# Kernel tuning notes

Hardware: AMD Instinct MI355X
Metric: run time of the kernel (lower is better)

Reference implementation:

```python
import jax, jax.numpy as jnp
import numpy as np
from jax.scipy.special import logsumexp

SEQ, BATCH, NUM_TAGS = 1024, 512, 64


def setup_inputs() -> dict:
    key = jax.random.key(0)
    k_em, k_tag, k_len, k_s, k_e, k_t = jax.random.split(key, 6)
    emissions = jax.random.normal(k_em, (SEQ, BATCH, NUM_TAGS), dtype=jnp.float32)
    tags = jax.random.randint(k_tag, (SEQ, BATCH), 0, NUM_TAGS, dtype=jnp.int64)
    # random sequence lengths in [1, SEQ]; mask[0] is guaranteed all ones
    lengths = jax.random.randint(k_len, (BATCH,), 1, SEQ + 1)
    mask = (jnp.arange(SEQ)[:, None] < lengths[None, :]).astype(jnp.int32)
    # CRF params: uniform(-0.1, 0.1) as in reset_parameters()
    u = lambda k, shape: jax.random.uniform(k, shape, jnp.float32, -0.1, 0.1)
    return {
        "emissions": emissions,
        "tags": tags,
        "mask": mask,
        "start_transitions": u(k_s, (NUM_TAGS,)),
        "end_transitions": u(k_e, (NUM_TAGS,)),
        "transitions": u(k_t, (NUM_TAGS, NUM_TAGS)),
    }


def _compute_score(emissions, tags, maskf, start_transitions, end_transitions, transitions):
    # emissions: (S,B,T), tags/maskf: (S,B)
    S, B = tags.shape
    em_scores = jnp.take_along_axis(emissions, tags[:, :, None], axis=2)[..., 0]  # (S,B)
    trans_scores = transitions[tags[:-1], tags[1:]]  # (S-1,B)
    score = start_transitions[tags[0]] + em_scores[0]
    score = score + jnp.sum((trans_scores + em_scores[1:]) * maskf[1:], axis=0)
    seq_ends = maskf.astype(jnp.int32).sum(axis=0) - 1  # (B,)
    last_tags = tags[seq_ends, jnp.arange(B)]
    return score + end_transitions[last_tags]


def _compute_normalizer(emissions, mask, start_transitions, end_transitions, transitions):
    # forward algorithm: sequential logsumexp scan over timesteps
    def step(score, x):  # score: (B,T)
        em_t, m_t = x  # (B,T), (B,)
        nxt = logsumexp(score[:, :, None] + transitions[None, :, :] + em_t[:, None, :], axis=1)
        score = jnp.where(m_t[:, None] > 0, nxt, score)
        return score, None

    score0 = start_transitions[None, :] + emissions[0]  # (B,T)
    score, _ = jax.lax.scan(step, score0, (emissions[1:], mask[1:]))
    return logsumexp(score + end_transitions[None, :], axis=1)  # (B,)


def reference(emissions, tags, mask, start_transitions, end_transitions, transitions):
    maskf = mask.astype(emissions.dtype)
    numerator = _compute_score(emissions, tags, maskf, start_transitions, end_transitions, transitions)
    denominator = _compute_normalizer(emissions, mask, start_transitions, end_transitions, transitions)
    llh = numerator - denominator
    return llh.sum()  # reduction='sum' (default)
```

## Files before the change

### kernel.cpp

```cpp
#include <hip/hip_runtime.h>
#include <stdint.h>

#define SEQ 1024
#define BATCH 512
#define NTAGS 64
#define HALF_T 512
#define LOGD 4.158883083f

typedef _Float16 v2h   __attribute__((ext_vector_type(2)));
typedef float    f32x4 __attribute__((ext_vector_type(4)));

__device__ __forceinline__ float dot2acc(v2h a, v2h b, float c) {
#if __has_builtin(__builtin_amdgcn_fdot2)
    return __builtin_amdgcn_fdot2(a, b, c, false);
#else
    return fmaf((float)a.x, (float)b.x, fmaf((float)a.y, (float)b.y, c));
#endif
}

__device__ __forceinline__ float rfl(float x) {
    return __uint_as_float(__builtin_amdgcn_readfirstlane(__float_as_uint(x)));
}

__device__ __forceinline__ v2h bch(float f) { return __builtin_bit_cast(v2h, f); }

__global__ __launch_bounds__(128)
void crf_kernel(const float* __restrict__ em,
                const int* __restrict__ tags,
                const int* __restrict__ mask,
                const float* __restrict__ startT,
                const float* __restrict__ endT,
                const float* __restrict__ trans,
                float* __restrict__ out)
{
    const int  b   = blockIdx.x;
    const int  wid = threadIdx.x >> 6;
    const int  j   = threadIdx.x & 63;
    const bool fwd = (wid == 0);

    __shared__ __align__(16) _Float16 bsh[2][NTAGS];
    __shared__ float gsh[NTAGS];
    __shared__ float mb_np[2];

    const unsigned lbase = (unsigned)(uintptr_t)(&bsh[wid][0]);
    const unsigned wa    = lbase + 2u * (unsigned)j;
    const unsigned ra    = lbase;

    int lsum = 0;
#pragma unroll
    for (int k = 0; k < SEQ / 64; ++k)
        lsum += mask[(k * 64 + j) * BATCH + b];
#pragma unroll
    for (int off = 32; off > 0; off >>= 1)
        lsum += __shfl_xor(lsum, off);
    const int L = lsum;

    v2h w[32];
#pragma unroll
    for (int i = 0; i < 32; ++i) {
        float a0, a1;
        if (fwd) { a0 = trans[(2 * i) * NTAGS + j]; a1 = trans[(2 * i + 1) * NTAGS + j]; }
        else     { a0 = trans[j * NTAGS + 2 * i];   a1 = trans[j * NTAGS + 2 * i + 1];   }
        v2h t; t.x = (_Float16)__expf(a0); t.y = (_Float16)__expf(a1);
        w[i] = t;
    }

#define DOT(WRVAL, SOUT)                                                         \
    {                                                                            \
        f32x4 q0, q1, q2, q3, q4, q5, q6, q7;                                    \
        float vtmp;                                                              \
        asm volatile(                                                            \
            "v_cvt_f16_f32 %[t], %[v]\n\t"                                       \
            "ds_write_b16 %[wa], %[t]\n\t"                                       \
            "ds_read_b128 %[a0], %[ra] offset:0\n\t"                             \
            "ds_read_b128 %[a1], %[ra] offset:16\n\t"                            \
            "ds_read_b128 %[a2], %[ra] offset:32\n\t"                            \
            "ds_read_b128 %[a3], %[ra] offset:48\n\t"                            \
            "ds_read_b128 %[a4], %[ra] offset:64\n\t"                            \
            "ds_read_b128 %[a5], %[ra] offset:80\n\t"                            \
            "ds_read_b128 %[a6], %[ra] offset:96\n\t"                            \
            "ds_read_b128 %[a7], %[ra] offset:112\n\t"                           \
            "s_waitcnt lgkmcnt(4)"                                               \
            : [a0] "=&v"(q0), [a1] "=&v"(q1), [a2] "=&v"(q2), [a3] "=&v"(q3),    \
              [a4] "=&v"(q4), [a5] "=&v"(q5), [a6] "=&v"(q6), [a7] "=&v"(q7),    \
              [t] "=&v"(vtmp)                                                    \
            : [v] "v"(WRVAL), [wa] "v"(wa), [ra] "v"(ra));                       \
        __builtin_amdgcn_sched_barrier(0);                                       \
        float s0 = 0.f, s1 = 0.f, s2 = 0.f, s3 = 0.f;                            \
        s0 = dot2acc(bch(q0.x), w[0],  s0);                                      \
        s1 = dot2acc(bch(q1.x), w[4],  s1);                                      \
        s2 = dot2acc(bch(q2.x), w[8],  s2);                                      \
        s3 = dot2acc(bch(q3.x), w[12], s3);                                      \
        s0 = dot2acc(bch(q0.y), w[1],  s0);                                      \
        s1 = dot2acc(bch(q1.y), w[5],  s1);                                      \
        s2 = dot2acc(bch(q2.y), w[9],  s2);                                      \
        s3 = dot2acc(bch(q3.y), w[13], s3);                                      \
        s0 = dot2acc(bch(q0.z), w[2],  s0);                                      \
        s1 = dot2acc(bch(q1.z), w[6],  s1);                                      \
        s2 = dot2acc(bch(q2.z), w[10], s2);                                      \
        s3 = dot2acc(bch(q3.z), w[14], s3);                                      \
        s0 = dot2acc(bch(q0.w), w[3],  s0);                                      \
        s1 = dot2acc(bch(q1.w), w[7],  s1);                                      \
        s2 = dot2acc(bch(q2.w), w[11], s2);                                      \
        s3 = dot2acc(bch(q3.w), w[15], s3);                                      \
        asm volatile("s_waitcnt lgkmcnt(0)"                                      \
                     : "+v"(q4), "+v"(q5), "+v"(q6), "+v"(q7));                  \
        __builtin_amdgcn_sched_barrier(0);                                       \
        float s4 = 0.f, s5 = 0.f, s6 = 0.f, s7 = 0.f;                            \
        s4 = dot2acc(bch(q4.x), w[16], s4);                                      \
        s5 = dot2acc(bch(q5.x), w[20], s5);                                      \
        s6 = dot2acc(bch(q6.x), w[24], s6);                                      \
        s7 = dot2acc(bch(q7.x), w[28], s7);                                      \
        s4 = dot2acc(bch(q4.y), w[17], s4);                                      \
        s5 = dot2acc(bch(q5.y), w[21], s5);                                      \
        s6 = dot2acc(bch(q6.y), w[25], s6);                                      \
        s7 = dot2acc(bch(q7.y), w[29], s7);                                      \
        s4 = dot2acc(bch(q4.z), w[18], s4);                                      \
        s5 = dot2acc(bch(q5.z), w[22], s5);                                      \
        s6 = dot2acc(bch(q6.z), w[26], s6);                                      \
        s7 = dot2acc(bch(q7.z), w[30], s7);                                      \
        s4 = dot2acc(bch(q4.w), w[19], s4);                                      \
        s5 = dot2acc(bch(q5.w), w[23], s5);                                      \
        s6 = dot2acc(bch(q6.w), w[27], s6);                                      \
        s7 = dot2acc(bch(q7.w), w[31], s7);                                      \
        SOUT = ((s0 + s1) + (s2 + s3)) + ((s4 + s5) + (s6 + s7));                \
    }

    float beta, M;
    int nsteps = 0;

    if (fwd) {
        float em0 = em[(size_t)b * NTAGS + j];
        float a0  = startT[j] + em0;
        M    = __shfl(a0, 0);
        beta = __expf(a0 - M);

        const int Lf = min(L - 1, HALF_T - 1);
        int t = 1;
        float cur[4], nxt[4];
#pragma unroll
        for (int u = 0; u < 4; ++u) {
            cur[u] = em[((size_t)min(t + u,     SEQ - 1) * BATCH + b) * NTAGS + j];
            nxt[u] = em[((size_t)min(t + 4 + u, SEQ - 1) * BATCH + b) * NTAGS + j];
        }
        while (t + 3 <= Lf) {
            float pre[4];
#pragma unroll
            for (int u = 0; u < 4; ++u)
                pre[u] = em[((size_t)min(t + 8 + u, SEQ - 1) * BATCH + b) * NTAGS + j];
            float eem[4];
#pragma unroll
            for (int u = 0; u < 4; ++u) eem[u] = __expf(cur[u] - LOGD);

            float s;
            DOT(beta, s); beta = s * eem[0];
            DOT(beta, s);
            float r = rfl(s);
            beta = s * eem[1];
            DOT(beta, s); beta = s * eem[2];
            float rinv = 1.0f / r;
            float lr   = __logf(r);
            DOT(beta, s); beta = s * (eem[3] * rinv);
            M += lr;
            nsteps += 4;
#pragma unroll
            for (int u = 0; u < 4; ++u) { cur[u] = nxt[u]; nxt[u] = pre[u]; }
            t += 4;
        }
        for (; t <= Lf; ++t) {
            float emt = em[((size_t)t * BATCH + b) * NTAGS + j];
            float s; DOT(beta, s);
            beta = s * __expf(emt - LOGD);
            ++nsteps;
        }
    } else {
        beta = __expf(endT[j]);
        M = 0.0f;
        if (L - 1 >= HALF_T) {
            int tt = L - 1;
            float cur[4], nxt[4];
#pragma unroll
            for (int u = 0; u < 4; ++u) {
                cur[u] = em[((size_t)max(tt - u,     0) * BATCH + b) * NTAGS + j];
                nxt[u] = em[((size_t)max(tt - 4 - u, 0) * BATCH + b) * NTAGS + j];
            }
            while (tt - 3 >= HALF_T) {
                float pre[4];
#pragma unroll
                for (int u = 0; u < 4; ++u)
                    pre[u] = em[((size_t)max(tt - 8 - u, 0) * BATCH + b) * NTAGS + j];
                float eem[4];
#pragma unroll
                for (int u = 0; u < 4; ++u) eem[u] = __expf(cur[u] - LOGD);

                float s;
                DOT(beta * eem[0], s); beta = s;
                DOT(beta * eem[1], s);
                float r = rfl(s);
                beta = s;
                DOT(beta * eem[2], s); beta = s;
                float rinv = 1.0f / r;
                float lr   = __logf(r);
                DOT(beta * (eem[3] * rinv), s); beta = s;
                M += lr;
                nsteps += 4;
#pragma unroll
                for (int u = 0; u < 4; ++u) { cur[u] = nxt[u]; nxt[u] = pre[u]; }
                tt -= 4;
            }
            for (; tt >= HALF_T; --tt) {
                float emt = em[((size_t)tt * BATCH + b) * NTAGS + j];
                float s; DOT(beta * __expf(emt - LOGD), s);
                beta = s;
                ++nsteps;
            }
        }
    }
#undef DOT

    const float Mfb = fmaf((float)nsteps, LOGD, M);

    if (!fwd) {
        gsh[j] = beta;
        if (j == 0) mb_np[0] = Mfb;
    }

    float np = 0.0f;
#pragma unroll
    for (int k = 0; k < SEQ / 128; ++k) {
        int t = k * 128 + wid * 64 + j;
        if (t >= 1 && t < L) {
            int ct = tags[t * BATCH + b];
            int pt = tags[(t - 1) * BATCH + b];
            np += trans[pt * NTAGS + ct] + em[((size_t)t * BATCH + b) * NTAGS + ct];
        }
    }
    if (threadIdx.x == 0) {
        int t0 = tags[b];
        np += startT[t0] + em[(size_t)b * NTAGS + t0]
            + endT[tags[(size_t)(L - 1) * BATCH + b]];
    }
#pragma unroll
    for (int off = 32; off > 0; off >>= 1)
        np += __shfl_xor(np, off);
    if (!fwd && j == 0) mb_np[1] = np;

    __syncthreads();

    if (fwd) {
        float p = beta * gsh[j];
#pragma unroll
        for (int off = 32; off > 0; off >>= 1)
            p += __shfl_xor(p, off);
        if (j == 0) {
            float denom = __logf(p) + Mfb + mb_np[0];
            atomicAdd(out, (np + mb_np[1]) - denom);
        }
    }
}

extern "C" void kernel_launch(void* const* d_in, const int* in_sizes, int n_in,
                              void* d_out, int out_size, void* d_ws, size_t ws_size,
                              hipStream_t stream)
{
    const float* em     = (const float*)d_in[0];
    const int*   tags   = (const int*)d_in[1];
    const int*   mask   = (const int*)d_in[2];
    const float* startT = (const float*)d_in[3];
    const float* endT   = (const float*)d_in[4];
    const float* trans  = (const float*)d_in[5];
    float*       out    = (float*)d_out;

    (void)d_ws; (void)ws_size;

    hipMemsetAsync(out, 0, sizeof(float) * out_size, stream);
    crf_kernel<<<BATCH, 128, 0, stream>>>(em, tags, mask, startT, endT, trans, out);
}
```

Baseline: 308.4 us.

## Replace LDS broadcast of alpha vector with cross-lane DPP/permlane expansion

The per-step all-to-all broadcast of the 64-wide scaled score vector, previously done with an LDS write and eight 128-bit LDS reads, now runs entirely in registers. It uses permlane32/16 swaps, packed fp16 conversion and a tree of DPP moves. Each lane gets its own permuted ordering of source tags, so the transition weights are loaded with a matching index permutation. This removes LDS latency and waits from the serial recurrence, at the cost of about 30 dependent DPP instructions per step and some extra register pressure.

Result: slower. 348.9 us (+13.1%).

```diff
diff --git a/kernel.cpp b/kernel.cpp
--- a/kernel.cpp
+++ b/kernel.cpp
@@ -1,5 +1,4 @@
 #include <hip/hip_runtime.h>
-#include <stdint.h>
 
 #define SEQ 1024
 #define BATCH 512
@@ -7,8 +6,7 @@
 #define HALF_T 512
 #define LOGD 4.158883083f
 
-typedef _Float16 v2h   __attribute__((ext_vector_type(2)));
-typedef float    f32x4 __attribute__((ext_vector_type(4)));
+typedef _Float16 v2h __attribute__((ext_vector_type(2)));
 
 __device__ __forceinline__ float dot2acc(v2h a, v2h b, float c) {
 #if __has_builtin(__builtin_amdgcn_fdot2)
@@ -22,7 +20,56 @@
     return __uint_as_float(__builtin_amdgcn_readfirstlane(__float_as_uint(x)));
 }
 
-__device__ __forceinline__ v2h bch(float f) { return __builtin_bit_cast(v2h, f); }
+template<int CTRL>
+__device__ __forceinline__ unsigned dppmov(unsigned v) {
+    return (unsigned)__builtin_amdgcn_mov_dpp((int)v, CTRL, 0xf, 0xf, false);
+}
+
+__device__ __forceinline__ void swap32pair(unsigned x, unsigned& a, unsigned& b) {
+#if __has_builtin(__builtin_amdgcn_permlane32_swap)
+    auto r = __builtin_amdgcn_permlane32_swap(x, x, false, false);
+    a = (unsigned)r[0]; b = (unsigned)r[1];
+#else
+    a = x; b = (unsigned)__shfl_xor((int)x, 32);
+#endif
+}
+
+__device__ __forceinline__ void swap16pair(unsigned x, unsigned& a, unsigned& b) {
+#if __has_builtin(__builtin_amdgcn_permlane16_swap)
+    auto r = __builtin_amdgcn_permlane16_swap(x, x, false, false);
+    a = (unsigned)r[0]; b = (unsigned)r[1];
+#else
+    a = x; b = (unsigned)__shfl_xor((int)x, 16);
+#endif
+}
+
+__device__ __forceinline__ void expand64(unsigned p0, unsigned u[32]) {
+    swap16pair(p0, u[0], u[1]);
+    u[2] = dppmov<0x140>(u[0]);
+    u[3] = dppmov<0x140>(u[1]);
+#pragma unroll
+    for (int k = 0; k < 4; ++k)  u[4 + k]  = dppmov<0x141>(u[k]);
+#pragma unroll
+    for (int k = 0; k < 8; ++k)  u[8 + k]  = dppmov<0x4E>(u[k]);
+#pragma unroll
+    for (int k = 0; k < 16; ++k) u[16 + k] = dppmov<0xB1>(u[k]);
+}
+
+__device__ __forceinline__ void bcast64(float x, v2h p[32]) {
+    unsigned a, b;
+    swap32pair(__float_as_uint(x), a, b);
+#if __has_builtin(__builtin_amdgcn_cvt_pkrtz)
+    auto pk_ = __builtin_amdgcn_cvt_pkrtz(__uint_as_float(a), __uint_as_float(b));
+    unsigned pk = __builtin_bit_cast(unsigned, pk_);
+#else
+    v2h pkv; pkv.x = (_Float16)__uint_as_float(a); pkv.y = (_Float16)__uint_as_float(b);
+    unsigned pk = __builtin_bit_cast(unsigned, pkv);
+#endif
+    unsigned u[32];
+    expand64(pk, u);
+#pragma unroll
+    for (int s = 0; s < 32; ++s) p[s] = __builtin_bit_cast(v2h, u[s]);
+}
 
 __global__ __launch_bounds__(128)
 void crf_kernel(const float* __restrict__ em,
@@ -38,13 +85,8 @@
     const int  j   = threadIdx.x & 63;
     const bool fwd = (wid == 0);
 
-    __shared__ __align__(16) _Float16 bsh[2][NTAGS];
     __shared__ float gsh[NTAGS];
     __shared__ float mb_np[2];
-
-    const unsigned lbase = (unsigned)(uintptr_t)(&bsh[wid][0]);
-    const unsigned wa    = lbase + 2u * (unsigned)j;
-    const unsigned ra    = lbase;
 
     int lsum = 0;
 #pragma unroll
@@ -55,75 +97,43 @@
         lsum += __shfl_xor(lsum, off);
     const int L = lsum;
 
+    unsigned I[32];
+    {
+        unsigned ia, ib;
+        swap32pair((unsigned)j, ia, ib);
+        unsigned i0 = (ia & 0xffffu) | (ib << 16);
+        expand64(i0, I);
+    }
+
     v2h w[32];
 #pragma unroll
-    for (int i = 0; i < 32; ++i) {
-        float a0, a1;
-        if (fwd) { a0 = trans[(2 * i) * NTAGS + j]; a1 = trans[(2 * i + 1) * NTAGS + j]; }
-        else     { a0 = trans[j * NTAGS + 2 * i];   a1 = trans[j * NTAGS + 2 * i + 1];   }
+    for (int s = 0; s < 32; ++s) {
+        unsigned i0 = I[s] & 0xffffu;
+        unsigned i1 = I[s] >> 16;
+        float a0 = fwd ? trans[i0 * NTAGS + j] : trans[j * NTAGS + i0];
+        float a1 = fwd ? trans[i1 * NTAGS + j] : trans[j * NTAGS + i1];
         v2h t; t.x = (_Float16)__expf(a0); t.y = (_Float16)__expf(a1);
-        w[i] = t;
-    }
-
-#define DOT(WRVAL, SOUT)                                                         \
-    {                                                                            \
-        f32x4 q0, q1, q2, q3, q4, q5, q6, q7;                                    \
-        float vtmp;                                                              \
-        asm volatile(                                                            \
-            "v_cvt_f16_f32 %[t], %[v]\n\t"                                       \
-            "ds_write_b16 %[wa], %[t]\n\t"                                       \
-            "ds_read_b128 %[a0], %[ra] offset:0\n\t"                             \
-            "ds_read_b128 %[a1], %[ra] offset:16\n\t"                            \
-            "ds_read_b128 %[a2], %[ra] offset:32\n\t"                            \
-            "ds_read_b128 %[a3], %[ra] offset:48\n\t"                            \
-            "ds_read_b128 %[a4], %[ra] offset:64\n\t"                            \
-            "ds_read_b128 %[a5], %[ra] offset:80\n\t"                            \
-            "ds_read_b128 %[a6], %[ra] offset:96\n\t"                            \
-            "ds_read_b128 %[a7], %[ra] offset:112\n\t"                           \
-            "s_waitcnt lgkmcnt(4)"                                               \
-            : [a0] "=&v"(q0), [a1] "=&v"(q1), [a2] "=&v"(q2), [a3] "=&v"(q3),    \
-              [a4] "=&v"(q4), [a5] "=&v"(q5), [a6] "=&v"(q6), [a7] "=&v"(q7),    \
-              [t] "=&v"(vtmp)                                                    \
-            : [v] "v"(WRVAL), [wa] "v"(wa), [ra] "v"(ra));                       \
-        __builtin_amdgcn_sched_barrier(0);                                       \
-        float s0 = 0.f, s1 = 0.f, s2 = 0.f, s3 = 0.f;                            \
-        s0 = dot2acc(bch(q0.x), w[0],  s0);                                      \
-        s1 = dot2acc(bch(q1.x), w[4],  s1);                                      \
-        s2 = dot2acc(bch(q2.x), w[8],  s2);                                      \
-        s3 = dot2acc(bch(q3.x), w[12], s3);                                      \
-        s0 = dot2acc(bch(q0.y), w[1],  s0);                                      \
-        s1 = dot2acc(bch(q1.y), w[5],  s1);                                      \
-        s2 = dot2acc(bch(q2.y), w[9],  s2);                                      \
-        s3 = dot2acc(bch(q3.y), w[13], s3);                                      \
-        s0 = dot2acc(bch(q0.z), w[2],  s0);                                      \
-        s1 = dot2acc(bch(q1.z), w[6],  s1);                                      \
-        s2 = dot2acc(bch(q2.z), w[10], s2);                                      \
-        s3 = dot2acc(bch(q3.z), w[14], s3);                                      \
-        s0 = dot2acc(bch(q0.w), w[3],  s0);                                      \
-        s1 = dot2acc(bch(q1.w), w[7],  s1);                                      \
-        s2 = dot2acc(bch(q2.w), w[11], s2);                                      \
-        s3 = dot2acc(bch(q3.w), w[15], s3);                                      \
-        asm volatile("s_waitcnt lgkmcnt(0)"                                      \
-                     : "+v"(q4), "+v"(q5), "+v"(q6), "+v"(q7));                  \
-        __builtin_amdgcn_sched_barrier(0);                                       \
-        float s4 = 0.f, s5 = 0.f, s6 = 0.f, s7 = 0.f;                            \
-        s4 = dot2acc(bch(q4.x), w[16], s4);                                      \
-        s5 = dot2acc(bch(q5.x), w[20], s5);                                      \
-        s6 = dot2acc(bch(q6.x), w[24], s6);                                      \
-        s7 = dot2acc(bch(q7.x), w[28], s7);                                      \
-        s4 = dot2acc(bch(q4.y), w[17], s4);                                      \
-        s5 = dot2acc(bch(q5.y), w[21], s5);                                      \
-        s6 = dot2acc(bch(q6.y), w[25], s6);                                      \
-        s7 = dot2acc(bch(q7.y), w[29], s7);                                      \
-        s4 = dot2acc(bch(q4.z), w[18], s4);                                      \
-        s5 = dot2acc(bch(q5.z), w[22], s5);                                      \
-        s6 = dot2acc(bch(q6.z), w[26], s6);                                      \
-        s7 = dot2acc(bch(q7.z), w[30], s7);                                      \
-        s4 = dot2acc(bch(q4.w), w[19], s4);                                      \
-        s5 = dot2acc(bch(q5.w), w[23], s5);                                      \
-        s6 = dot2acc(bch(q6.w), w[27], s6);                                      \
-        s7 = dot2acc(bch(q7.w), w[31], s7);                                      \
-        SOUT = ((s0 + s1) + (s2 + s3)) + ((s4 + s5) + (s6 + s7));                \
+        w[s] = t;
+    }
+
+#define DOT(WRVAL, SOUT)                                                   \
+    {                                                                      \
+        v2h p_[32];                                                        \
+        bcast64((WRVAL), p_);                                              \
+        float s0 = 0.f, s1 = 0.f, s2 = 0.f, s3 = 0.f;                      \
+        float s4 = 0.f, s5 = 0.f, s6 = 0.f, s7 = 0.f;                      \
+        _Pragma("unroll")                                                  \
+        for (int q = 0; q < 4; ++q) {                                      \
+            s0 = dot2acc(p_[8 * q + 0], w[8 * q + 0], s0);                 \
+            s1 = dot2acc(p_[8 * q + 1], w[8 * q + 1], s1);                 \
+            s2 = dot2acc(p_[8 * q + 2], w[8 * q + 2], s2);                 \
+            s3 = dot2acc(p_[8 * q + 3], w[8 * q + 3], s3);                 \
+            s4 = dot2acc(p_[8 * q + 4], w[8 * q + 4], s4);                 \
+            s5 = dot2acc(p_[8 * q + 5], w[8 * q + 5], s5);                 \
+            s6 = dot2acc(p_[8 * q + 6], w[8 * q + 6], s6);                 \
+            s7 = dot2acc(p_[8 * q + 7], w[8 * q + 7], s7);                 \
+        }                                                                  \
+        SOUT = ((s0 + s1) + (s2 + s3)) + ((s4 + s5) + (s6 + s7));          \
     }
 
     float beta, M;
```
